# Optimization experiments

Measured on AMD Instinct MI355X. Metric: run time of the kernel, lower is better.

Reference implementation:

```python
import jax, jax.numpy as jnp
import numpy as np

N, E, L, D = 4, 64, 512, 768


def setup_inputs() -> dict:
    key = jax.random.key(0)
    k1, k2, k3, k4 = jax.random.split(key, 4)
    doc_state = jax.random.normal(k1, (N, L, D), dtype=jnp.float32)
    # 0/1 entity membership mask, float as in the torch module's multiply
    entity_mapping = jax.random.randint(k2, (N, E, L), 0, 2).astype(jnp.float32)
    # lens consistent with the mask; clamp to >=1 to avoid divide-by-zero
    entity_lens = jnp.maximum(entity_mapping.sum(axis=-1), 1.0)
    W = jax.random.normal(k3, (D, 2 * D), dtype=jnp.float32) * 0.02  # torch Linear weight [out, in]
    b = jnp.zeros((D,), dtype=jnp.float32)
    return {"doc_state": doc_state, "entity_mapping": entity_mapping,
            "entity_lens": entity_lens, "W": W, "b": b}


def reference(doc_state, entity_mapping, entity_lens, W, b):
    # entity_states: N x E x L x d (the large broadcast intermediate)
    entity_states = entity_mapping[:, :, :, None] * doc_state[:, None, :, :]
    max_pooled = jnp.max(entity_states, axis=2)                      # N x E x d
    mean_pooled = jnp.sum(entity_states, axis=2) / entity_lens[:, :, None]  # N x E x d
    output = jnp.concatenate([max_pooled, mean_pooled], axis=2)      # N x E x 2d
    return jnp.einsum('nek,dk->ned', output, W) + b                  # N x E x d
```

## Files before the change

kernel.cpp:

```cpp
#include <hip/hip_runtime.h>
#include <hip/hip_bf16.h>
#include <math.h>

#define PN 4
#define PE 64
#define PL 512
#define PD 768
#define PK2 (2 * PD)
#define PM (PN * PE)

#define EG 4
#define DCW 64
#define NDC (PD / DCW)
#define NPOOLB (PN * (PE / EG) * NDC)
#define NCVT 288
#define NXCD 8

using bf16x8 = __attribute__((ext_vector_type(8))) short;
using f32x4  = __attribute__((ext_vector_type(4))) float;

static __device__ __forceinline__ unsigned short f2bf(float x) {
    unsigned int u = __float_as_uint(x);
    unsigned int r = (u + 0x7FFFu + ((u >> 16) & 1u)) >> 16;
    return (unsigned short)r;
}

__global__ __launch_bounds__(512) void pool_v6(
    const float* __restrict__ doc,
    const float* __restrict__ map,
    const float* __restrict__ lens,
    const float* __restrict__ W,
    unsigned short* __restrict__ Pb,
    unsigned short* __restrict__ Wb)
{
    const int bid = blockIdx.x;
    const int tid = threadIdx.x;
    const int xcd = bid & (NXCD - 1);
    const int idx = bid >> 3;

    if (idx >= 96) {
        const int ci = xcd * 36 + (idx - 96);
        const size_t i = ((size_t)ci * 512 + tid) * 8;
        const float4 a = *reinterpret_cast<const float4*>(W + i);
        const float4 c = *reinterpret_cast<const float4*>(W + i + 4);
        union { unsigned short s[8]; uint4 v; } r;
        r.s[0] = f2bf(a.x); r.s[1] = f2bf(a.y); r.s[2] = f2bf(a.z); r.s[3] = f2bf(a.w);
        r.s[4] = f2bf(c.x); r.s[5] = f2bf(c.y); r.s[6] = f2bf(c.z); r.s[7] = f2bf(c.w);
        *reinterpret_cast<uint4*>(Wb + i) = r.v;
        return;
    }

    __shared__ float lmax[8][EG][64];
    __shared__ float lsum[8][EG][64];

    const int n   = xcd >> 1;
    const int dh  = xcd & 1;
    const int eg  = idx / 6;
    const int dc  = dh * 6 + (idx % 6);
    const int e0  = eg * EG;
    const int d0  = dc * DCW;
    const int w    = tid >> 6;
    const int lane = tid & 63;

    unsigned long long mk[EG];
    #pragma unroll
    for (int e = 0; e < EG; ++e) {
        const float m = map[((size_t)n * PE + e0 + e) * PL + w * 64 + lane];
        mk[e] = __ballot(m != 0.0f);
    }

    const float* docp = doc + ((size_t)n * PL + w * 64) * PD + d0 + lane;

    float mx[EG], sm[EG];
    #pragma unroll
    for (int e = 0; e < EG; ++e) { mx[e] = -INFINITY; sm[e] = 0.f; }

    #pragma unroll 16
    for (int l = 0; l < 64; ++l) {
        const float v = docp[(size_t)l * PD];
        #pragma unroll
        for (int e = 0; e < EG; ++e) {
            const float mval = ((mk[e] >> l) & 1ull) ? 1.0f : 0.0f;
            const float cand = mval * v;
            sm[e] += cand;
            mx[e] = fmaxf(mx[e], cand);
        }
    }

    #pragma unroll
    for (int e = 0; e < EG; ++e) {
        lmax[w][e][lane] = mx[e];
        lsum[w][e][lane] = sm[e];
    }
    __syncthreads();

    const int slot = tid & 255;
    const int e  = slot >> 6;
    const int ln = slot & 63;
    const int ne = n * PE + e0 + e;
    const int d  = d0 + ln;
    if (tid < 256) {
        float m = lmax[0][e][ln];
        #pragma unroll
        for (int ww = 1; ww < 8; ++ww) m = fmaxf(m, lmax[ww][e][ln]);
        Pb[(size_t)ne * PK2 + d] = f2bf(m);
    } else {
        float s = lsum[0][e][ln];
        #pragma unroll
        for (int ww = 1; ww < 8; ++ww) s += lsum[ww][e][ln];
        Pb[(size_t)ne * PK2 + PD + d] = f2bf(s * (1.0f / lens[ne]));
    }
}

__global__ __launch_bounds__(128) void gemm_ks2x(
    const unsigned short* __restrict__ Pb,
    const unsigned short* __restrict__ Wb,
    const float* __restrict__ b,
    float* __restrict__ out)
{
    __shared__ f32x4 red[64];

    const int w    = threadIdx.x >> 6;
    const int lane = threadIdx.x & 63;
    const int bid  = blockIdx.x;
    const int xcd  = bid & (NXCD - 1);
    const int idx  = bid >> 3;
    const int ct = xcd * 6 + (idx >> 4);
    const int rt = idx & 15;
    const int r0 = rt * 16, d0 = ct * 16;

    const int fr = lane & 15;
    const int kg = lane >> 4;
    const int kb = w * (PK2 / 2);

    const unsigned short* pA = Pb + (size_t)(r0 + fr) * PK2 + kb + kg * 8;
    const unsigned short* pB = Wb + (size_t)(d0 + fr) * PK2 + kb + kg * 8;

    f32x4 acc0 = {0.f, 0.f, 0.f, 0.f};
    f32x4 acc1 = {0.f, 0.f, 0.f, 0.f};
    #pragma unroll
    for (int k0 = 0; k0 < PK2 / 2; k0 += 64) {
        const bf16x8 a0 = *reinterpret_cast<const bf16x8*>(pA + k0);
        const bf16x8 b0 = *reinterpret_cast<const bf16x8*>(pB + k0);
        acc0 = __builtin_amdgcn_mfma_f32_16x16x32_bf16(a0, b0, acc0, 0, 0, 0);
        const bf16x8 a1 = *reinterpret_cast<const bf16x8*>(pA + k0 + 32);
        const bf16x8 b1 = *reinterpret_cast<const bf16x8*>(pB + k0 + 32);
        acc1 = __builtin_amdgcn_mfma_f32_16x16x32_bf16(a1, b1, acc1, 0, 0, 0);
    }
    f32x4 acc = acc0 + acc1;

    if (w == 1) red[lane] = acc;
    __syncthreads();
    if (w == 0) {
        acc += red[lane];
        const int c = d0 + fr;
        const float bias = b[c];
        #pragma unroll
        for (int j = 0; j < 4; ++j)
            out[(size_t)(r0 + kg * 4 + j) * PD + c] = acc[j] + bias;
    }
}

__global__ __launch_bounds__(256) void fused_kernel(
    const float* __restrict__ doc, const float* __restrict__ map,
    const float* __restrict__ lens, const float* __restrict__ W,
    const float* __restrict__ b, float* __restrict__ out)
{
    __shared__ float Prow[PK2];
    const int ne = blockIdx.x, n = ne >> 6, t = threadIdx.x;
    const float* docn = doc + (size_t)n * PL * PD;
    const float* mrow = map + (size_t)ne * PL;
    float mx0=-INFINITY, mx1=-INFINITY, mx2=-INFINITY, s0=0.f, s1=0.f, s2=0.f;
    bool has_zero = false;
    for (int l = 0; l < PL; ++l) {
        const float m = mrow[l];
        if (m != 0.0f) {
            const float* dr = docn + (size_t)l * PD;
            const float a = dr[t], c = dr[t+256], e = dr[t+512];
            mx0=fmaxf(mx0,a); s0+=a; mx1=fmaxf(mx1,c); s1+=c; mx2=fmaxf(mx2,e); s2+=e;
        } else has_zero = true;
    }
    if (has_zero) { mx0=fmaxf(mx0,0.f); mx1=fmaxf(mx1,0.f); mx2=fmaxf(mx2,0.f); }
    const float invlen = 1.0f / lens[ne];
    Prow[t]=mx0; Prow[t+256]=mx1; Prow[t+512]=mx2;
    Prow[PD+t]=s0*invlen; Prow[PD+t+256]=s1*invlen; Prow[PD+t+512]=s2*invlen;
    __syncthreads();
    #pragma unroll
    for (int i = 0; i < 3; ++i) {
        const int d = t + i*256;
        const float* wrow = W + (size_t)d * PK2;
        float acc = 0.f;
        for (int k = 0; k < PK2; k += 4) {
            const float4 w = *reinterpret_cast<const float4*>(&wrow[k]);
            acc += Prow[k]*w.x + Prow[k+1]*w.y + Prow[k+2]*w.z + Prow[k+3]*w.w;
        }
        out[(size_t)ne * PD + d] = acc + b[d];
    }
}

extern "C" void kernel_launch(void* const* d_in, const int* in_sizes, int n_in,
                              void* d_out, int out_size, void* d_ws, size_t ws_size,
                              hipStream_t stream) {
    const float* doc  = (const float*)d_in[0];
    const float* map  = (const float*)d_in[1];
    const float* lens = (const float*)d_in[2];
    const float* W    = (const float*)d_in[3];
    const float* b    = (const float*)d_in[4];
    float* out = (float*)d_out;

    const size_t pb_bytes = (size_t)PM * PK2 * sizeof(unsigned short);
    const size_t wb_bytes = (size_t)PD * PK2 * sizeof(unsigned short);
    const size_t need     = pb_bytes + wb_bytes;

    if (ws_size >= need) {
        unsigned short* Pb = (unsigned short*)d_ws;
        unsigned short* Wb = (unsigned short*)((char*)d_ws + pb_bytes);
        pool_v6<<<dim3(NPOOLB + NCVT), dim3(512), 0, stream>>>(
            doc, map, lens, W, Pb, Wb);
        gemm_ks2x<<<dim3((PM / 16) * (PD / 16)), dim3(128), 0, stream>>>(Pb, Wb, b, out);
    } else {
        fused_kernel<<<dim3(PM), dim3(256), 0, stream>>>(doc, map, lens, W, b, out);
    }
}
```

Before: 28.60 us.

## Compute mean pooling as bf16 MFMA matmul of mask and doc

Moves the masked-sum (mean pooling) out of the scalar pooling loop into separate blocks that treat it as a matrix product of the 0/1 mask and the document, evaluated with bf16 MFMA instructions. The max-pooling path keeps only the max reduction, which drops half the shared memory and the sum reduction. The doc values are rounded to bf16 before accumulation, which adds rounding error compared with the fp32 sum. The new blocks load doc with strided per-lane column reads, which may be poorly coalesced.

```diff
diff --git a/kernel.cpp b/kernel.cpp
--- a/kernel.cpp
+++ b/kernel.cpp
@@ -12,9 +12,9 @@
 #define EG 4
 #define DCW 64
 #define NDC (PD / DCW)
-#define NPOOLB (PN * (PE / EG) * NDC)
-#define NCVT 288
 #define NXCD 8
+#define NPW 1056
+#define NMG 96
 
 using bf16x8 = __attribute__((ext_vector_type(8))) short;
 using f32x4  = __attribute__((ext_vector_type(4))) float;
@@ -25,7 +25,7 @@
     return (unsigned short)r;
 }
 
-__global__ __launch_bounds__(512) void pool_v6(
+__global__ __launch_bounds__(512) void k1_pool_mean(
     const float* __restrict__ doc,
     const float* __restrict__ map,
     const float* __restrict__ lens,
@@ -33,8 +33,52 @@
     unsigned short* __restrict__ Pb,
     unsigned short* __restrict__ Wb)
 {
-    const int bid = blockIdx.x;
-    const int tid = threadIdx.x;
+    const int bid  = blockIdx.x;
+    const int tid  = threadIdx.x;
+    const int w    = tid >> 6;
+    const int lane = tid & 63;
+
+    if (bid >= NPW) {
+        const int t  = (bid - NPW) * 8 + w;
+        const int ct = t % 48;
+        const int rq = (t / 48) & 3;
+        const int n  = t / 192;
+        const int r0 = rq * 16;
+        const int d0 = ct * 16;
+        const int fr = lane & 15;
+        const int kg = lane >> 4;
+
+        const float* mrow = map + ((size_t)n * PE + r0 + fr) * PL + kg * 8;
+        const float* dcol = doc + (size_t)n * PL * PD + d0 + fr;
+
+        f32x4 acc = {0.f, 0.f, 0.f, 0.f};
+        for (int k0 = 0; k0 < PL; k0 += 32) {
+            const float4 ma = *reinterpret_cast<const float4*>(mrow + k0);
+            const float4 mb = *reinterpret_cast<const float4*>(mrow + k0 + 4);
+            union { unsigned short s[8]; bf16x8 v; } af;
+            af.s[0] = (ma.x != 0.f) ? 0x3F80 : 0;
+            af.s[1] = (ma.y != 0.f) ? 0x3F80 : 0;
+            af.s[2] = (ma.z != 0.f) ? 0x3F80 : 0;
+            af.s[3] = (ma.w != 0.f) ? 0x3F80 : 0;
+            af.s[4] = (mb.x != 0.f) ? 0x3F80 : 0;
+            af.s[5] = (mb.y != 0.f) ? 0x3F80 : 0;
+            af.s[6] = (mb.z != 0.f) ? 0x3F80 : 0;
+            af.s[7] = (mb.w != 0.f) ? 0x3F80 : 0;
+            union { unsigned short s[8]; bf16x8 v; } bfr;
+            #pragma unroll
+            for (int j = 0; j < 8; ++j)
+                bfr.s[j] = f2bf(dcol[(size_t)(k0 + kg * 8 + j) * PD]);
+            acc = __builtin_amdgcn_mfma_f32_16x16x32_bf16(af.v, bfr.v, acc, 0, 0, 0);
+        }
+        const int d = d0 + fr;
+        #pragma unroll
+        for (int j = 0; j < 4; ++j) {
+            const int ne = n * PE + r0 + kg * 4 + j;
+            Pb[(size_t)ne * PK2 + PD + d] = f2bf(acc[j] / lens[ne]);
+        }
+        return;
+    }
+
     const int xcd = bid & (NXCD - 1);
     const int idx = bid >> 3;
 
@@ -51,7 +95,6 @@
     }
 
     __shared__ float lmax[8][EG][64];
-    __shared__ float lsum[8][EG][64];
 
     const int n   = xcd >> 1;
     const int dh  = xcd & 1;
@@ -59,8 +102,6 @@
     const int dc  = dh * 6 + (idx % 6);
     const int e0  = eg * EG;
     const int d0  = dc * DCW;
-    const int w    = tid >> 6;
-    const int lane = tid & 63;
 
     unsigned long long mk[EG];
     #pragma unroll
@@ -71,9 +112,9 @@
 
     const float* docp = doc + ((size_t)n * PL + w * 64) * PD + d0 + lane;
 
-    float mx[EG], sm[EG];
-    #pragma unroll
-    for (int e = 0; e < EG; ++e) { mx[e] = -INFINITY; sm[e] = 0.f; }
+    float mx[EG];
+    #pragma unroll
+    for (int e = 0; e < EG; ++e) mx[e] = -INFINITY;
 
     #pragma unroll 16
     for (int l = 0; l < 64; ++l) {
@@ -81,34 +122,22 @@
         #pragma unroll
         for (int e = 0; e < EG; ++e) {
             const float mval = ((mk[e] >> l) & 1ull) ? 1.0f : 0.0f;
-            const float cand = mval * v;
-            sm[e] += cand;
-            mx[e] = fmaxf(mx[e], cand);
-        }
-    }
-
-    #pragma unroll
-    for (int e = 0; e < EG; ++e) {
-        lmax[w][e][lane] = mx[e];
-        lsum[w][e][lane] = sm[e];
-    }
+            mx[e] = fmaxf(mx[e], mval * v);
+        }
+    }
+
+    #pragma unroll
+    for (int e = 0; e < EG; ++e) lmax[w][e][lane] = mx[e];
     __syncthreads();
 
-    const int slot = tid & 255;
-    const int e  = slot >> 6;
-    const int ln = slot & 63;
-    const int ne = n * PE + e0 + e;
-    const int d  = d0 + ln;
     if (tid < 256) {
+        const int e  = tid >> 6;
+        const int ln = tid & 63;
+        const int ne = n * PE + e0 + e;
         float m = lmax[0][e][ln];
         #pragma unroll
         for (int ww = 1; ww < 8; ++ww) m = fmaxf(m, lmax[ww][e][ln]);
-        Pb[(size_t)ne * PK2 + d] = f2bf(m);
-    } else {
-        float s = lsum[0][e][ln];
-        #pragma unroll
-        for (int ww = 1; ww < 8; ++ww) s += lsum[ww][e][ln];
-        Pb[(size_t)ne * PK2 + PD + d] = f2bf(s * (1.0f / lens[ne]));
+        Pb[(size_t)ne * PK2 + d0 + ln] = f2bf(m);
     }
 }
 
@@ -215,7 +244,7 @@
     if (ws_size >= need) {
         unsigned short* Pb = (unsigned short*)d_ws;
         unsigned short* Wb = (unsigned short*)((char*)d_ws + pb_bytes);
-        pool_v6<<<dim3(NPOOLB + NCVT), dim3(512), 0, stream>>>(
+        k1_pool_mean<<<dim3(NPW + NMG), dim3(512), 0, stream>>>(
             doc, map, lens, W, Pb, Wb);
         gemm_ks2x<<<dim3((PM / 16) * (PD / 16)), dim3(128), 0, stream>>>(Pb, Wb, b, out);
     } else {
```

After: 36.28 us. +26.8%, slower.

## Widen pooling tiles to 256 columns with float4 loads and 1024-thread blocks

Applied to the files above, without the earlier changes.

The pooling kernel now uses 1024-thread blocks. Each wave covers 32 sequence rows and each lane covers 4 columns through float4 loads, and each block handles a 256-column slice instead of 64. This cuts the pooling grid from 768 blocks to 192 and aims to improve load width and per-thread work. The cross-wave reduction now goes through one reused shared buffer in two passes with extra barriers. With fewer blocks the kernel risks underfilling the GPU, and the larger per-thread register state may limit occupancy.

```diff
diff --git a/kernel.cpp b/kernel.cpp
--- a/kernel.cpp
+++ b/kernel.cpp
@@ -10,10 +10,9 @@
 #define PM (PN * PE)
 
 #define EG 4
-#define DCW 64
-#define NDC (PD / DCW)
-#define NPOOLB (PN * (PE / EG) * NDC)
-#define NCVT 288
+#define DCW 256
+#define NPOOLB 192
+#define NCVT2 144
 #define NXCD 8
 
 using bf16x8 = __attribute__((ext_vector_type(8))) short;
@@ -25,7 +24,7 @@
     return (unsigned short)r;
 }
 
-__global__ __launch_bounds__(512) void pool_v6(
+__global__ __launch_bounds__(1024) void pool_v10(
     const float* __restrict__ doc,
     const float* __restrict__ map,
     const float* __restrict__ lens,
@@ -35,12 +34,9 @@
 {
     const int bid = blockIdx.x;
     const int tid = threadIdx.x;
-    const int xcd = bid & (NXCD - 1);
-    const int idx = bid >> 3;
-
-    if (idx >= 96) {
-        const int ci = xcd * 36 + (idx - 96);
-        const size_t i = ((size_t)ci * 512 + tid) * 8;
+
+    if (bid >= NPOOLB) {
+        const size_t i = ((size_t)(bid - NPOOLB) * 1024 + tid) * 8;
         const float4 a = *reinterpret_cast<const float4*>(W + i);
         const float4 c = *reinterpret_cast<const float4*>(W + i + 4);
         union { unsigned short s[8]; uint4 v; } r;
@@ -50,65 +46,75 @@
         return;
     }
 
-    __shared__ float lmax[8][EG][64];
-    __shared__ float lsum[8][EG][64];
-
+    __shared__ float lbuf[16][EG][DCW];
+
+    const int xcd = bid & (NXCD - 1);
+    const int idx = bid >> 3;
     const int n   = xcd >> 1;
-    const int dh  = xcd & 1;
-    const int eg  = idx / 6;
-    const int dc  = dh * 6 + (idx % 6);
+    const int eg  = (xcd & 1) * 8 + idx / 3;
+    const int dc  = idx % 3;
     const int e0  = eg * EG;
     const int d0  = dc * DCW;
     const int w    = tid >> 6;
     const int lane = tid & 63;
 
-    unsigned long long mk[EG];
+    unsigned int mk[EG];
     #pragma unroll
     for (int e = 0; e < EG; ++e) {
-        const float m = map[((size_t)n * PE + e0 + e) * PL + w * 64 + lane];
-        mk[e] = __ballot(m != 0.0f);
-    }
-
-    const float* docp = doc + ((size_t)n * PL + w * 64) * PD + d0 + lane;
-
-    float mx[EG], sm[EG];
-    #pragma unroll
-    for (int e = 0; e < EG; ++e) { mx[e] = -INFINITY; sm[e] = 0.f; }
-
-    #pragma unroll 16
-    for (int l = 0; l < 64; ++l) {
-        const float v = docp[(size_t)l * PD];
+        const float m = map[((size_t)n * PE + e0 + e) * PL + w * 32 + (lane & 31)];
+        mk[e] = (unsigned int)__ballot(m != 0.0f);
+    }
+
+    const float* docp = doc + ((size_t)n * PL + w * 32) * PD + d0 + lane * 4;
+
+    float4 mx[EG], sm[EG];
+    #pragma unroll
+    for (int e = 0; e < EG; ++e) {
+        mx[e] = make_float4(-INFINITY, -INFINITY, -INFINITY, -INFINITY);
+        sm[e] = make_float4(0.f, 0.f, 0.f, 0.f);
+    }
+
+    #pragma unroll 8
+    for (int l = 0; l < 32; ++l) {
+        const float4 v = *reinterpret_cast<const float4*>(docp + (size_t)l * PD);
         #pragma unroll
         for (int e = 0; e < EG; ++e) {
-            const float mval = ((mk[e] >> l) & 1ull) ? 1.0f : 0.0f;
-            const float cand = mval * v;
-            sm[e] += cand;
-            mx[e] = fmaxf(mx[e], cand);
+            const float mval = ((mk[e] >> l) & 1u) ? 1.0f : 0.0f;
+            const float cx = mval * v.x, cy = mval * v.y;
+            const float cz = mval * v.z, cw = mval * v.w;
+            sm[e].x += cx; sm[e].y += cy; sm[e].z += cz; sm[e].w += cw;
+            mx[e].x = fmaxf(mx[e].x, cx); mx[e].y = fmaxf(mx[e].y, cy);
+            mx[e].z = fmaxf(mx[e].z, cz); mx[e].w = fmaxf(mx[e].w, cw);
         }
     }
 
     #pragma unroll
-    for (int e = 0; e < EG; ++e) {
-        lmax[w][e][lane] = mx[e];
-        lsum[w][e][lane] = sm[e];
-    }
-    __syncthreads();
-
-    const int slot = tid & 255;
-    const int e  = slot >> 6;
-    const int ln = slot & 63;
-    const int ne = n * PE + e0 + e;
-    const int d  = d0 + ln;
-    if (tid < 256) {
-        float m = lmax[0][e][ln];
-        #pragma unroll
-        for (int ww = 1; ww < 8; ++ww) m = fmaxf(m, lmax[ww][e][ln]);
-        Pb[(size_t)ne * PK2 + d] = f2bf(m);
-    } else {
-        float s = lsum[0][e][ln];
-        #pragma unroll
-        for (int ww = 1; ww < 8; ++ww) s += lsum[ww][e][ln];
-        Pb[(size_t)ne * PK2 + PD + d] = f2bf(s * (1.0f / lens[ne]));
+    for (int e = 0; e < EG; ++e)
+        *reinterpret_cast<float4*>(&lbuf[w][e][lane * 4]) = mx[e];
+    __syncthreads();
+    {
+        const int e = tid >> 8;
+        const int d = tid & 255;
+        float m = lbuf[0][e][d];
+        #pragma unroll
+        for (int ww = 1; ww < 16; ++ww) m = fmaxf(m, lbuf[ww][e][d]);
+        const int ne = n * PE + e0 + e;
+        Pb[(size_t)ne * PK2 + d0 + d] = f2bf(m);
+    }
+    __syncthreads();
+
+    #pragma unroll
+    for (int e = 0; e < EG; ++e)
+        *reinterpret_cast<float4*>(&lbuf[w][e][lane * 4]) = sm[e];
+    __syncthreads();
+    {
+        const int e = tid >> 8;
+        const int d = tid & 255;
+        float s = lbuf[0][e][d];
+        #pragma unroll
+        for (int ww = 1; ww < 16; ++ww) s += lbuf[ww][e][d];
+        const int ne = n * PE + e0 + e;
+        Pb[(size_t)ne * PK2 + PD + d0 + d] = f2bf(s * (1.0f / lens[ne]));
     }
 }
 
@@ -215,7 +221,7 @@
     if (ws_size >= need) {
         unsigned short* Pb = (unsigned short*)d_ws;
         unsigned short* Wb = (unsigned short*)((char*)d_ws + pb_bytes);
-        pool_v6<<<dim3(NPOOLB + NCVT), dim3(512), 0, stream>>>(
+        pool_v10<<<dim3(NPOOLB + NCVT2), dim3(1024), 0, stream>>>(
             doc, map, lens, W, Pb, Wb);
         gemm_ks2x<<<dim3((PM / 16) * (PD / 16)), dim3(128), 0, stream>>>(Pb, Wb, b, out);
     } else {
```

Result: faster. 26.64 us, median of 2 (-6.8%).
